# Kernel optimization log

Hardware: AMD Instinct MI355X
Metric: run time of the kernel (lower is better)

The kernel has to match this reference:

```python
import jax, jax.numpy as jnp
import numpy as np

B, N, D, E = 128, 512, 256, 8192  # graphs, nodes/graph, embed_dim, edges/graph
K = int(np.ceil(0.8 * N))         # TopKPooling ratio=0.8 -> k per graph


def setup_inputs() -> dict:
    key = jax.random.key(0)
    ks = jax.random.split(key, 16)
    Ntot = B * N
    x = jax.random.normal(ks[0], (Ntot, 4), jnp.float32)
    offs = (jnp.arange(B, dtype=jnp.int32) * N)[:, None]
    src = (jax.random.randint(ks[1], (B, E), 0, N, jnp.int32) + offs).reshape(-1)
    dst = (jax.random.randint(ks[2], (B, E), 0, N, jnp.int32) + offs).reshape(-1)
    s = 0.05
    w = lambda k, shape: jax.random.normal(k, shape, jnp.float32) * s
    return {
        'x': x, 'src': src, 'dst': dst,
        'Wr1': w(ks[3], (4, D)), 'Ws1': w(ks[4], (4, D)), 'b1': jnp.zeros((D,), jnp.float32),
        'Wr2': w(ks[5], (D, D)), 'Ws2': w(ks[6], (D, D)), 'b2': jnp.zeros((D,), jnp.float32),
        'Wr3': w(ks[7], (D, D)), 'Ws3': w(ks[8], (D, D)), 'b3': jnp.zeros((D,), jnp.float32),
        'p_attn': w(ks[9], (D,)),
        'W1': w(ks[10], (2 * D, D)), 'c1': jnp.zeros((D,), jnp.float32),
        'W2': w(ks[11], (D, D // 2)), 'c2': jnp.zeros((D // 2,), jnp.float32),
        'W3': w(ks[12], (D // 2, 1)), 'c3': jnp.zeros((1,), jnp.float32),
    }


def _graph_conv(x, src, dst, Wr, Ws, b):
    # PyG GraphConv, aggr='add': out = lin_rel(sum_{j in N(i)} x_j) + lin_root(x_i)
    agg = jax.ops.segment_sum(x[src], dst, num_segments=B * N)
    return agg @ Wr + b + x @ Ws


def _gmp_gap(xb):
    # xb: [B, n, D] -> concat(global max pool, global mean pool): [B, 2D]
    return jnp.concatenate([xb.max(axis=1), xb.mean(axis=1)], axis=1)


def reference(x, src, dst, Wr1, Ws1, b1, Wr2, Ws2, b2, Wr3, Ws3, b3,
              p_attn, W1, c1, W2, c2, W3, c3):
    h = jax.nn.relu(_graph_conv(x, src, dst, Wr1, Ws1, b1))
    x1 = _gmp_gap(h.reshape(B, N, D))
    h = jax.nn.relu(_graph_conv(h, src, dst, Wr2, Ws2, b2))
    x2 = _gmp_gap(h.reshape(B, N, D))
    h = jax.nn.relu(_graph_conv(h, src, dst, Wr3, Ws3, b3))
    # TopKPooling: score = x.p/||p||; keep top-k per graph; scale by tanh(score)
    score = (h @ p_attn) / (jnp.linalg.norm(p_attn) + 1e-16)
    vals, idx = jax.lax.top_k(score.reshape(B, N), K)           # [B, K]
    hb = h.reshape(B, N, D)
    sel = jnp.take_along_axis(hb, idx[:, :, None], axis=1) * jnp.tanh(vals)[:, :, None]
    x3 = _gmp_gap(sel)
    z = x1 + x2 + x3
    z = jax.nn.relu(z @ W1 + c1)
    z = jax.nn.relu(z @ W2 + c2)  # dropout is identity in eval mode
    return jax.nn.sigmoid(z @ W3 + c3)[:, 0]
```

## Files before the change

### kernel.cpp

```cpp
#include <hip/hip_runtime.h>

typedef unsigned short u16;
typedef unsigned int u32;

#define B_GRAPHS 128
#define N_NODES  512
#define D_DIM    256
#define E_EDGES  8192
#define K_TOP    410
#define CSR_STRIDE 12288
#define AS 132

typedef __attribute__((ext_vector_type(8))) __bf16 bf16x8;
typedef __attribute__((ext_vector_type(4))) float  f32x4;

__device__ __forceinline__ float bf2f(u16 h) {
  union { u32 u; float f; } c; c.u = ((u32)h) << 16; return c.f;
}
__device__ __forceinline__ float u2f(u32 u) {
  union { u32 u; float f; } c; c.u = u; return c.f;
}
__device__ __forceinline__ u16 f2bf(float f) {
  union { float f; u32 u; } c; c.f = f;
  u32 u = c.u;
  u += 0x7fffu + ((u >> 16) & 1u);
  return (u16)(u >> 16);
}
__device__ __forceinline__ void async_copy16(const void* g, void* l) {
  __builtin_amdgcn_global_load_lds((const __attribute__((address_space(1))) void*)g,
                                   (__attribute__((address_space(3))) void*)l, 16, 0, 0);
}

__global__ void zero_kernel(float* __restrict__ p) {
  *(float4*)&p[(size_t)(blockIdx.x * 256 + threadIdx.x) * 4] = float4{0.f, 0.f, 0.f, 0.f};
}

__global__ void prep_kernel(const float* __restrict__ Wr2, const float* __restrict__ Ws2,
                            const float* __restrict__ Wr3, const float* __restrict__ Ws3,
                            u16* __restrict__ WT) {
  const int mat = blockIdx.y;
  const int n = blockIdx.x;
  const int k = threadIdx.x;
  const float* W = (mat == 0) ? Wr2 : (mat == 1) ? Ws2 : (mat == 2) ? Wr3 : Ws3;
  WT[((size_t)mat << 16) + ((size_t)n << 8) + k] = f2bf(W[(size_t)k * 256 + n]);
}

__global__ __launch_bounds__(256) void csr_kernel(const int* __restrict__ src,
                                                  const int* __restrict__ dst,
                                                  u16* __restrict__ csr_col,
                                                  u32* __restrict__ csr_off) {
  __shared__ u32 cnt[512];
  __shared__ u32 scan[512];
  __shared__ u32 poff[513];
  const int g = blockIdx.x, t = threadIdx.x;
  const int base = g * N_NODES, ebase = g * E_EDGES;
  for (int i = t; i < 512; i += 256) cnt[i] = 0;
  __syncthreads();
  for (int e = t; e < E_EDGES; e += 256)
    atomicAdd(&cnt[dst[ebase + e] - base], 1u);
  __syncthreads();
  for (int i = t; i < 512; i += 256) scan[i] = (cnt[i] + 7u) & ~7u;
  __syncthreads();
  #pragma unroll 1
  for (int d = 1; d < 512; d <<= 1) {
    const u32 v0 = (t >= d) ? scan[t - d] : 0u;
    const u32 v1 = scan[t + 256 - d];
    __syncthreads();
    if (t >= d) scan[t] += v0;
    scan[t + 256] += v1;
    __syncthreads();
  }
  if (t == 0) poff[0] = 0;
  for (int i = t; i < 512; i += 256) poff[i + 1] = scan[i];
  __syncthreads();
  for (int i = t; i < 513; i += 256) csr_off[(size_t)g * 513 + i] = poff[i];
  for (int i = t; i < 512; i += 256) {
    const u32 s = poff[i] + cnt[i], e2 = poff[i + 1];
    for (u32 k = s; k < e2; ++k) csr_col[(size_t)g * CSR_STRIDE + k] = 512;
  }
  __syncthreads();
  for (int i = t; i < 512; i += 256) cnt[i] = poff[i];
  __syncthreads();
  for (int e = t; e < E_EDGES; e += 256) {
    const int d = dst[ebase + e] - base;
    const int s = src[ebase + e] - base;
    const u32 pos = atomicAdd(&cnt[d], 1u);
    csr_col[(size_t)g * CSR_STRIDE + pos] = (u16)s;
  }
}

__global__ __launch_bounds__(256) void conv1_kernel(const float* __restrict__ x,
                             const u16* __restrict__ csr_col, const u32* __restrict__ csr_off,
                             const float* __restrict__ Wr1, const float* __restrict__ Ws1,
                             const float* __restrict__ b1,
                             u16* __restrict__ H1, float* __restrict__ X1) {
  __shared__ float xs[513 * 4];
  __shared__ float aggs[N_NODES * 5];
  __shared__ __align__(16) u16 cols[CSR_STRIDE];
  __shared__ u32 offs[513];
  const int c = blockIdx.x;
  const int g = blockIdx.y;
  const int base = g * N_NODES;
  const int t = threadIdx.x;

  for (int i = t; i < N_NODES; i += 256)
    *(float4*)&xs[i * 4] = *(const float4*)&x[(size_t)(base + i) * 4];
  if (t < 4) xs[512 * 4 + t] = 0.f;
  for (int i = t; i < CSR_STRIDE / 2; i += 256)
    ((u32*)cols)[i] = ((const u32*)(csr_col + (size_t)g * CSR_STRIDE))[i];
  for (int i = t; i < 513; i += 256) offs[i] = csr_off[(size_t)g * 513 + i];
  __syncthreads();

  #pragma unroll
  for (int nn = 0; nn < 2; ++nn) {
    const int i = t * 2 + nn;
    const u32 s0 = offs[i];
    const int nb = (int)((offs[i + 1] - s0) >> 3);
    float a0 = 0.f, a1 = 0.f, a2 = 0.f, a3 = 0.f;
    for (int b = 0; b < nb; ++b) {
      const uint4 cw = *(const uint4*)&cols[s0 + (u32)b * 8];
      const u32 ww[4] = {cw.x, cw.y, cw.z, cw.w};
      #pragma unroll
      for (int q = 0; q < 4; ++q) {
        const int ca = ww[q] & 0xffffu, cb = ww[q] >> 16;
        const float4 va = *(const float4*)&xs[ca * 4];
        const float4 vb = *(const float4*)&xs[cb * 4];
        a0 += va.x + vb.x; a1 += va.y + vb.y;
        a2 += va.z + vb.z; a3 += va.w + vb.w;
      }
    }
    aggs[i * 5 + 0] = a0; aggs[i * 5 + 1] = a1;
    aggs[i * 5 + 2] = a2; aggs[i * 5 + 3] = a3;
  }
  __syncthreads();

  float wr[4], wsv[4];
  #pragma unroll
  for (int k = 0; k < 4; ++k) { wr[k] = Wr1[k * 256 + t]; wsv[k] = Ws1[k * 256 + t]; }
  const float bb = b1[t];
  float mx = 0.f, sm = 0.f;
  const int nlo = c * 256;
  for (int n = nlo; n < nlo + 256; ++n) {
    float acc = bb;
    #pragma unroll
    for (int k = 0; k < 4; ++k) acc += aggs[n * 5 + k] * wr[k] + xs[n * 4 + k] * wsv[k];
    acc = fmaxf(acc, 0.f);
    H1[(size_t)(base + n) * D_DIM + t] = f2bf(acc);
    mx = fmaxf(mx, acc);
    sm += acc;
  }
  atomicMax((int*)&X1[(size_t)g * 512 + t], __float_as_int(mx));
  atomicAdd(&X1[(size_t)g * 512 + 256 + t], sm);
}

__global__ __launch_bounds__(512) void agg_gather_kernel(const u16* __restrict__ H,
                                                         const u16* __restrict__ csr_col,
                                                         const u32* __restrict__ csr_off,
                                                         u16* __restrict__ AGG) {
  __shared__ __align__(16) u16 hs[513 * AS];
  __shared__ __align__(16) u16 cols[CSR_STRIDE + 8];
  __shared__ u32 offs[513];
  const int c = blockIdx.x;
  const int g = blockIdx.y;
  const int base = g * N_NODES;
  const int t = threadIdx.x;

  #pragma unroll
  for (int p = 0; p < 32; ++p) {
    const int flat = p * 512 + t;
    const int row = flat >> 5, q = flat & 31;
    *(uint2*)&hs[row * AS + q * 4] =
        *(const uint2*)&H[(size_t)(base + row) * D_DIM + c * 128 + q * 4];
  }
  if (t < 33) *(uint2*)&hs[512 * AS + t * 4] = uint2{0u, 0u};
  #pragma unroll
  for (int p = 0; p < 12; ++p)
    ((u32*)cols)[p * 512 + t] = ((const u32*)(csr_col + (size_t)g * CSR_STRIDE))[p * 512 + t];
  if (t < 8) cols[CSR_STRIDE + t] = 512;
  for (int i = t; i < 513; i += 512) offs[i] = csr_off[(size_t)g * 513 + i];
  __syncthreads();

  const int w = t >> 6, lane = t & 63;
  const int h2 = lane >> 5, fl = lane & 31;
  const int i0 = w * 64;
  #pragma unroll 1
  for (int j = 0; j < 16; ++j) {
    u32 s0[4]; int nb[4];
    #pragma unroll
    for (int q = 0; q < 4; ++q) {
      const int r = i0 + q * 16 + j;
      s0[q] = offs[r];
      nb[q] = (int)((offs[r + 1] - s0[q]) >> 3);
    }
    const int nbmax = max(max(nb[0], nb[1]), max(nb[2], nb[3]));
    float a[4][4];
    #pragma unroll
    for (int q = 0; q < 4; ++q) { a[q][0] = 0.f; a[q][1] = 0.f; a[q][2] = 0.f; a[q][3] = 0.f; }
    #pragma unroll 1
    for (int b = 0; b < nbmax; ++b) {
      #pragma unroll
      for (int q = 0; q < 4; ++q) {
        const u32 ca = (b < nb[q]) ? (s0[q] + (u32)b * 8u) : (u32)CSR_STRIDE;
        const uint4 cw = *(const uint4*)&cols[ca];
        const u32 w01 = h2 ? cw.z : cw.x;
        const u32 w23 = h2 ? cw.w : cw.y;
        const int c0 = (int)(w01 & 0xffffu), c1 = (int)(w01 >> 16);
        const int c2 = (int)(w23 & 0xffffu), c3 = (int)(w23 >> 16);
        const uint2 d0 = *(const uint2*)&hs[c0 * AS + fl * 4];
        const uint2 d1 = *(const uint2*)&hs[c1 * AS + fl * 4];
        const uint2 d2 = *(const uint2*)&hs[c2 * AS + fl * 4];
        const uint2 d3 = *(const uint2*)&hs[c3 * AS + fl * 4];
        a[q][0] += (u2f(d0.x << 16) + u2f(d1.x << 16)) + (u2f(d2.x << 16) + u2f(d3.x << 16));
        a[q][1] += (u2f(d0.x & 0xffff0000u) + u2f(d1.x & 0xffff0000u))
                 + (u2f(d2.x & 0xffff0000u) + u2f(d3.x & 0xffff0000u));
        a[q][2] += (u2f(d0.y << 16) + u2f(d1.y << 16)) + (u2f(d2.y << 16) + u2f(d3.y << 16));
        a[q][3] += (u2f(d0.y & 0xffff0000u) + u2f(d1.y & 0xffff0000u))
                 + (u2f(d2.y & 0xffff0000u) + u2f(d3.y & 0xffff0000u));
      }
    }
    #pragma unroll
    for (int q = 0; q < 4; ++q) {
      const float r0 = a[q][0] + __shfl_xor(a[q][0], 32);
      const float r1 = a[q][1] + __shfl_xor(a[q][1], 32);
      const float r2 = a[q][2] + __shfl_xor(a[q][2], 32);
      const float r3 = a[q][3] + __shfl_xor(a[q][3], 32);
      if (h2 == 0) {
        uint2 o;
        o.x = (u32)f2bf(r0) | ((u32)f2bf(r1) << 16);
        o.y = (u32)f2bf(r2) | ((u32)f2bf(r3) << 16);
        *(uint2*)&AGG[(size_t)(base + i0 + q * 16 + j) * D_DIM + c * 128 + fl * 4] = o;
      }
    }
  }
}

__global__ __launch_bounds__(256) void gemm_kernel(const u16* __restrict__ Amat,
                                                   const u16* __restrict__ Hmat,
                                                   const u16* __restrict__ WrT,
                                                   const u16* __restrict__ WsT,
                                                   const float* __restrict__ bias,
                                                   u16* __restrict__ Hout,
                                                   float* __restrict__ x2pool,
                                                   float* __restrict__ score,
                                                   const float* __restrict__ pvec) {
  __shared__ __align__(16) u16 At[2][128 * 32];
  __shared__ __align__(16) u16 Bt[2][128 * 32];
  const int m0 = blockIdx.x * 128;
  const int n0 = blockIdx.y * 128;
  const int t = threadIdx.x;
  const int wid = t >> 6, lane = t & 63;
  const int wm = wid >> 1, wn = wid & 1;
  const int r16 = lane & 15, q0 = lane >> 4;

  f32x4 acc[4][4];
  const f32x4 zero = {0.f, 0.f, 0.f, 0.f};
  #pragma unroll
  for (int i = 0; i < 4; ++i)
    #pragma unroll
    for (int jj = 0; jj < 4; ++jj) acc[i][jj] = zero;

  const int srow_off = lane >> 2;
  const int sq = lane & 3;

  auto stage = [&](int s) {
    const int buf = s & 1;
    const int ph = s >> 3;
    const int kk = (s & 7) * 32;
    const u16* Ain = ph ? Hmat : Amat;
    const u16* Win = ph ? WsT : WrT;
    #pragma unroll
    for (int j = 0; j < 4; ++j) {
      const int chk = wid * 4 + j;
      const int ch8 = chk & 7;
      const int r = ch8 * 16 + srow_off;
      const int qsrc = sq ^ ((r >> 1) & 3);
      if (chk < 8)
        async_copy16(&Ain[(size_t)(m0 + r) * 256 + kk + qsrc * 8], &At[buf][ch8 * 512]);
      else
        async_copy16(&Win[(size_t)(n0 + r) * 256 + kk + qsrc * 8], &Bt[buf][ch8 * 512]);
    }
  };

  stage(0);
  #pragma unroll 1
  for (int s = 0; s < 16; ++s) {
    if (s < 15) {
      stage(s + 1);
      asm volatile("s_waitcnt vmcnt(4)" ::: "memory");
    } else {
      asm volatile("s_waitcnt vmcnt(0)" ::: "memory");
    }
    __builtin_amdgcn_s_barrier();
    const int buf = s & 1;
    bf16x8 aF[4], bF[4];
    #pragma unroll
    for (int mi = 0; mi < 4; ++mi) {
      const int arow = wm * 64 + mi * 16 + r16;
      const int qs = q0 ^ ((arow >> 1) & 3);
      aF[mi] = *(const bf16x8*)&At[buf][arow * 32 + qs * 8];
    }
    #pragma unroll
    for (int ni = 0; ni < 4; ++ni) {
      const int brow = wn * 64 + ni * 16 + r16;
      const int qs = q0 ^ ((brow >> 1) & 3);
      bF[ni] = *(const bf16x8*)&Bt[buf][brow * 32 + qs * 8];
    }
    #pragma unroll
    for (int mi = 0; mi < 4; ++mi)
      #pragma unroll
      for (int ni = 0; ni < 4; ++ni)
        acc[mi][ni] = __builtin_amdgcn_mfma_f32_16x16x32_bf16(aF[mi], bF[ni],
                                                              acc[mi][ni], 0, 0, 0);
    __builtin_amdgcn_s_barrier();
  }

  const bool do_x2 = (x2pool != nullptr);
  const bool do_sc = (score != nullptr);
  float colmax[4], colsum[4], pv[4], rpart[4][4];
  #pragma unroll
  for (int ni = 0; ni < 4; ++ni) { colmax[ni] = 0.f; colsum[ni] = 0.f; pv[ni] = 0.f; }
  #pragma unroll
  for (int mi = 0; mi < 4; ++mi)
    #pragma unroll
    for (int r = 0; r < 4; ++r) rpart[mi][r] = 0.f;
  if (do_sc) {
    #pragma unroll
    for (int ni = 0; ni < 4; ++ni) pv[ni] = pvec[n0 + wn * 64 + ni * 16 + r16];
  }

  #pragma unroll
  for (int mi = 0; mi < 4; ++mi) {
    const int growb = m0 + wm * 64 + mi * 16 + q0 * 4;
    #pragma unroll
    for (int ni = 0; ni < 4; ++ni) {
      const int gcol = n0 + wn * 64 + ni * 16 + r16;
      const float bv = bias[gcol];
      #pragma unroll
      for (int r = 0; r < 4; ++r) {
        float v = acc[mi][ni][r] + bv;
        v = fmaxf(v, 0.f);
        Hout[(size_t)(growb + r) * 256 + gcol] = f2bf(v);
        colmax[ni] = fmaxf(colmax[ni], v);
        colsum[ni] += v;
        rpart[mi][r] += v * pv[ni];
      }
    }
  }

  const int gg = m0 >> 9;
  if (do_x2) {
    #pragma unroll
    for (int ni = 0; ni < 4; ++ni) {
      const int gcol = n0 + wn * 64 + ni * 16 + r16;
      float cm = colmax[ni], cs = colsum[ni];
      cm = fmaxf(cm, __shfl_xor(cm, 16));
      cm = fmaxf(cm, __shfl_xor(cm, 32));
      cs += __shfl_xor(cs, 16);
      cs += __shfl_xor(cs, 32);
      if (q0 == 0) {
        atomicMax((int*)&x2pool[(size_t)gg * 512 + gcol], __float_as_int(cm));
        atomicAdd(&x2pool[(size_t)gg * 512 + 256 + gcol], cs);
      }
    }
  }
  if (do_sc) {
    #pragma unroll
    for (int mi = 0; mi < 4; ++mi) {
      const int growb = m0 + wm * 64 + mi * 16 + q0 * 4;
      #pragma unroll
      for (int r = 0; r < 4; ++r) {
        float sp = rpart[mi][r];
        sp += __shfl_xor(sp, 1);
        sp += __shfl_xor(sp, 2);
        sp += __shfl_xor(sp, 4);
        sp += __shfl_xor(sp, 8);
        if (r16 == 0) atomicAdd(&score[growb + r], sp);
      }
    }
  }
}

__global__ __launch_bounds__(256) void sort_kernel(const float* __restrict__ score,
                                                   const float* __restrict__ p,
                                                   u16* __restrict__ top_idx,
                                                   float* __restrict__ top_scale) {
  __shared__ float sval[N_NODES];
  __shared__ int sidx[N_NODES];
  __shared__ float wsum[4];
  const int g = blockIdx.x, t = threadIdx.x;

  float pvt = p[t];
  float sq2 = pvt * pvt;
  #pragma unroll
  for (int off = 32; off > 0; off >>= 1) sq2 += __shfl_down(sq2, off);
  if ((t & 63) == 0) wsum[t >> 6] = sq2;
  __syncthreads();
  const float inv_pn = 1.f / (sqrtf(wsum[0] + wsum[1] + wsum[2] + wsum[3]) + 1e-16f);

  for (int n = t; n < N_NODES; n += 256) {
    sval[n] = score[(size_t)g * 512 + n] * inv_pn;
    sidx[n] = n;
  }
  __syncthreads();

  for (int k = 2; k <= N_NODES; k <<= 1) {
    for (int jj = k >> 1; jj > 0; jj >>= 1) {
      const int i = ((t & ~(jj - 1)) << 1) | (t & (jj - 1));
      const int ix = i | jj;
      const bool dirDesc = ((i & k) == 0);
      const float vi = sval[i], vx = sval[ix];
      const int ii = sidx[i], ij = sidx[ix];
      const bool iAfter = (vi < vx) || (vi == vx && ii > ij);
      if (dirDesc ? iAfter : !iAfter) {
        sval[i] = vx; sval[ix] = vi;
        sidx[i] = ij; sidx[ix] = ii;
      }
      __syncthreads();
    }
  }

  for (int s = t; s < K_TOP; s += 256) {
    top_idx[(size_t)g * 416 + s] = (u16)sidx[s];
    top_scale[(size_t)g * 416 + s] = tanhf(sval[s]);
  }
}

__global__ __launch_bounds__(256) void x3_pool_kernel(const u16* __restrict__ H3,
                                                      const u16* __restrict__ top_idx,
                                                      const float* __restrict__ top_scale,
                                                      float* __restrict__ X3) {
  __shared__ u16 sidxL[416];
  __shared__ float ssclL[416];
  __shared__ float redm[32 * 65];
  __shared__ float reds[32 * 65];
  const int c = blockIdx.x;
  const int g = blockIdx.y;
  const int t = threadIdx.x;
  const int fl = t & 7, rg = t >> 3;

  for (int s = t; s < K_TOP; s += 256) {
    sidxL[s] = top_idx[(size_t)g * 416 + s];
    ssclL[s] = top_scale[(size_t)g * 416 + s];
  }
  __syncthreads();

  float mx[8], sm[8];
  #pragma unroll
  for (int j = 0; j < 8; ++j) { mx[j] = -1e30f; sm[j] = 0.f; }
  const size_t rowbase = (size_t)g * 512;
  for (int s = rg; s < K_TOP; s += 32) {
    const int row = sidxL[s];
    const float sc = ssclL[s];
    const uint4 d = *(const uint4*)&H3[(rowbase + row) * 256 + c * 64 + fl * 8];
    const u32 wv[4] = {d.x, d.y, d.z, d.w};
    #pragma unroll
    for (int q = 0; q < 4; ++q) {
      const float v0 = u2f(wv[q] << 16) * sc;
      const float v1 = u2f(wv[q] & 0xffff0000u) * sc;
      mx[q * 2] = fmaxf(mx[q * 2], v0); sm[q * 2] += v0;
      mx[q * 2 + 1] = fmaxf(mx[q * 2 + 1], v1); sm[q * 2 + 1] += v1;
    }
  }
  #pragma unroll
  for (int j = 0; j < 8; ++j) {
    redm[rg * 65 + fl * 8 + j] = mx[j];
    reds[rg * 65 + fl * 8 + j] = sm[j];
  }
  __syncthreads();
  for (int st = 16; st >= 1; st >>= 1) {
    if (rg < st) {
      #pragma unroll
      for (int j = 0; j < 8; ++j) {
        const int a = rg * 65 + fl * 8 + j, b = (rg + st) * 65 + fl * 8 + j;
        redm[a] = fmaxf(redm[a], redm[b]);
        reds[a] += reds[b];
      }
    }
    __syncthreads();
  }
  if (rg == 0) {
    #pragma unroll
    for (int j = 0; j < 8; ++j) {
      X3[(size_t)g * 512 + c * 64 + fl * 8 + j] = redm[fl * 8 + j];
      X3[(size_t)g * 512 + 256 + c * 64 + fl * 8 + j] = reds[fl * 8 + j] * (1.f / (float)K_TOP);
    }
  }
}

__global__ void mlp_kernel(const float* __restrict__ X1, const float* __restrict__ X2,
                           const float* __restrict__ X3,
                           const float* __restrict__ W1, const float* __restrict__ c1,
                           const float* __restrict__ W2, const float* __restrict__ c2,
                           const float* __restrict__ W3, const float* __restrict__ c3,
                           float* __restrict__ out) {
  __shared__ float zs[512];
  __shared__ float z1[256];
  __shared__ float z2[128];
  const int g = blockIdx.x, t = threadIdx.x;
  for (int k = t; k < 512; k += 256) {
    const float x1v = X1[(size_t)g * 512 + k];
    const float x2v = X2[(size_t)g * 512 + k];
    const float x3v = X3[(size_t)g * 512 + k];
    zs[k] = (k < 256) ? (x1v + x2v + x3v)
                      : (x1v * (1.f / 512.f) + x2v * (1.f / 512.f) + x3v);
  }
  __syncthreads();
  {
    float acc = c1[t];
    for (int k = 0; k < 512; ++k) acc += zs[k] * W1[(size_t)k * 256 + t];
    z1[t] = fmaxf(acc, 0.f);
  }
  __syncthreads();
  if (t < 128) {
    float acc = c2[t];
    for (int d = 0; d < 256; ++d) acc += z1[d] * W2[(size_t)d * 128 + t];
    z2[t] = fmaxf(acc, 0.f);
  }
  __syncthreads();
  if (t == 0) {
    float acc = c3[0];
    for (int e = 0; e < 128; ++e) acc += z2[e] * W3[e];
    out[g] = 1.f / (1.f + expf(-acc));
  }
}

extern "C" void kernel_launch(void* const* d_in, const int* in_sizes, int n_in,
                              void* d_out, int out_size, void* d_ws, size_t ws_size,
                              hipStream_t stream) {
  (void)in_sizes; (void)n_in; (void)out_size; (void)ws_size;
  const float* x   = (const float*)d_in[0];
  const int* src   = (const int*)d_in[1];
  const int* dstp  = (const int*)d_in[2];
  const float* Wr1 = (const float*)d_in[3];
  const float* Ws1 = (const float*)d_in[4];
  const float* b1  = (const float*)d_in[5];
  const float* Wr2 = (const float*)d_in[6];
  const float* Ws2 = (const float*)d_in[7];
  const float* b2  = (const float*)d_in[8];
  const float* Wr3 = (const float*)d_in[9];
  const float* Ws3 = (const float*)d_in[10];
  const float* b3  = (const float*)d_in[11];
  const float* pat = (const float*)d_in[12];
  const float* W1  = (const float*)d_in[13];
  const float* c1  = (const float*)d_in[14];
  const float* W2  = (const float*)d_in[15];
  const float* c2  = (const float*)d_in[16];
  const float* W3  = (const float*)d_in[17];
  const float* c3  = (const float*)d_in[18];
  float* out = (float*)d_out;

  char* ws = (char*)d_ws;
  u16* hA  = (u16*)(ws);
  u16* hB  = (u16*)(ws + 33554432);
  u16* AGG = (u16*)(ws + 67108864);
  u16* WT  = (u16*)(ws + 100663296);
  float* x1 = (float*)(ws + 101187584);
  float* x2 = (float*)(ws + 101449728);
  float* x3 = (float*)(ws + 101711872);
  u16* csr_col = (u16*)(ws + 101974016);
  u32* csr_off = (u32*)(ws + 105119744);
  float* score     = (float*)(ws + 101974016);
  u16* top_idx     = (u16*)(ws + 101974016 + 262144);
  float* top_scale = (float*)(ws + 101974016 + 372736);

  prep_kernel<<<dim3(256, 4), dim3(256), 0, stream>>>(Wr2, Ws2, Wr3, Ws3, WT);
  csr_kernel<<<dim3(128), dim3(256), 0, stream>>>(src, dstp, csr_col, csr_off);
  zero_kernel<<<dim3(128), dim3(256), 0, stream>>>(x1);
  conv1_kernel<<<dim3(2, 128), dim3(256), 0, stream>>>(x, csr_col, csr_off, Wr1, Ws1, b1, hA, x1);

  agg_gather_kernel<<<dim3(2, 128), dim3(512), 0, stream>>>(hA, csr_col, csr_off, AGG);
  gemm_kernel<<<dim3(512, 2), dim3(256), 0, stream>>>(AGG, hA, WT, WT + 65536, b2, hB,
                                                      x2, nullptr, nullptr);

  agg_gather_kernel<<<dim3(2, 128), dim3(512), 0, stream>>>(hB, csr_col, csr_off, AGG);
  zero_kernel<<<dim3(64), dim3(256), 0, stream>>>(score);
  gemm_kernel<<<dim3(512, 2), dim3(256), 0, stream>>>(AGG, hB, WT + 131072, WT + 196608, b3, hA,
                                                      nullptr, score, pat);

  sort_kernel<<<dim3(128), dim3(256), 0, stream>>>(score, pat, top_idx, top_scale);
  x3_pool_kernel<<<dim3(4, 128), dim3(256), 0, stream>>>(hA, top_idx, top_scale, x3);
  mlp_kernel<<<dim3(128), dim3(256), 0, stream>>>(x1, x2, x3, W1, c1, W2, c2, W3, c3, out);
}
```

Measured before the change: 267.1 us.

## Sort rows by degree per wave and prescale CSR column indices

CSR column entries now hold the source index premultiplied by 33 (AS/4), so the gather computes LDS addresses with a single add and shift instead of a multiply. conv1 decodes the index with a multiply-shift. Each wave bitonic-sorts its 64 rows by block count so the four rows handled together have similar degree, which cuts idle iterations from degree imbalance. The column buffer is shrunk to fit alongside the new sort workspace. This relies on the maximum padded edge count per graph fitting within LCOL, an assumption about the input distribution.

```diff
diff --git a/kernel.cpp b/kernel.cpp
--- a/kernel.cpp
+++ b/kernel.cpp
@@ -9,6 +9,7 @@
 #define E_EDGES  8192
 #define K_TOP    410
 #define CSR_STRIDE 12288
+#define LCOL 11792
 #define AS 132
 
 typedef __attribute__((ext_vector_type(8))) __bf16 bf16x8;
@@ -76,7 +77,7 @@
   for (int i = t; i < 513; i += 256) csr_off[(size_t)g * 513 + i] = poff[i];
   for (int i = t; i < 512; i += 256) {
     const u32 s = poff[i] + cnt[i], e2 = poff[i + 1];
-    for (u32 k = s; k < e2; ++k) csr_col[(size_t)g * CSR_STRIDE + k] = 512;
+    for (u32 k = s; k < e2; ++k) csr_col[(size_t)g * CSR_STRIDE + k] = 16896;
   }
   __syncthreads();
   for (int i = t; i < 512; i += 256) cnt[i] = poff[i];
@@ -85,7 +86,7 @@
     const int d = dst[ebase + e] - base;
     const int s = src[ebase + e] - base;
     const u32 pos = atomicAdd(&cnt[d], 1u);
-    csr_col[(size_t)g * CSR_STRIDE + pos] = (u16)s;
+    csr_col[(size_t)g * CSR_STRIDE + pos] = (u16)(s * 33);
   }
 }
 
@@ -122,7 +123,8 @@
       const u32 ww[4] = {cw.x, cw.y, cw.z, cw.w};
       #pragma unroll
       for (int q = 0; q < 4; ++q) {
-        const int ca = ww[q] & 0xffffu, cb = ww[q] >> 16;
+        const int ca = (int)(((ww[q] & 0xffffu) * 63551u) >> 21);
+        const int cb = (int)(((ww[q] >> 16) * 63551u) >> 21);
         const float4 va = *(const float4*)&xs[ca * 4];
         const float4 vb = *(const float4*)&xs[cb * 4];
         a0 += va.x + vb.x; a1 += va.y + vb.y;
@@ -158,8 +160,9 @@
                                                          const u32* __restrict__ csr_off,
                                                          u16* __restrict__ AGG) {
   __shared__ __align__(16) u16 hs[513 * AS];
-  __shared__ __align__(16) u16 cols[CSR_STRIDE + 8];
+  __shared__ __align__(16) u16 cols[LCOL];
   __shared__ u32 offs[513];
+  __shared__ u32 swork[512];
   const int c = blockIdx.x;
   const int g = blockIdx.y;
   const int base = g * N_NODES;
@@ -173,43 +176,72 @@
         *(const uint2*)&H[(size_t)(base + row) * D_DIM + c * 128 + q * 4];
   }
   if (t < 33) *(uint2*)&hs[512 * AS + t * 4] = uint2{0u, 0u};
-  #pragma unroll
-  for (int p = 0; p < 12; ++p)
-    ((u32*)cols)[p * 512 + t] = ((const u32*)(csr_col + (size_t)g * CSR_STRIDE))[p * 512 + t];
-  if (t < 8) cols[CSR_STRIDE + t] = 512;
+  {
+    const u32* colsw = (const u32*)(csr_col + (size_t)g * CSR_STRIDE);
+    #pragma unroll
+    for (int p = 0; p < 12; ++p) {
+      const int i = p * 512 + t;
+      if (i < (LCOL - 8) / 2) ((u32*)cols)[i] = colsw[i];
+    }
+  }
+  if (t < 8) cols[LCOL - 8 + t] = 16896;
   for (int i = t; i < 513; i += 512) offs[i] = csr_off[(size_t)g * 513 + i];
   __syncthreads();
 
   const int w = t >> 6, lane = t & 63;
+  {
+    const int row = (w << 6) + lane;
+    const u32 s0 = offs[row];
+    const u32 nb = (offs[row + 1] - s0) >> 3;
+    u32 key = (nb << 16) | (u32)row;
+    #pragma unroll
+    for (int k = 2; k <= 64; k <<= 1) {
+      #pragma unroll
+      for (int jj = k >> 1; jj > 0; jj >>= 1) {
+        const u32 o = (u32)__shfl_xor((int)key, jj);
+        const bool up = ((lane & k) == 0);
+        const bool lower = ((lane & jj) == 0);
+        const u32 mn = min(key, o), mx = max(key, o);
+        key = (up == lower) ? mn : mx;
+      }
+    }
+    swork[(w << 6) + lane] = key;
+  }
+  __syncthreads();
+
   const int h2 = lane >> 5, fl = lane & 31;
-  const int i0 = w * 64;
+  const int i0w = w << 6;
+  const u32 padu = (u32)(LCOL - 8 + h2 * 4);
+  const u32 h2o = (u32)(h2 * 4);
   #pragma unroll 1
   for (int j = 0; j < 16; ++j) {
-    u32 s0[4]; int nb[4];
-    #pragma unroll
-    for (int q = 0; q < 4; ++q) {
-      const int r = i0 + q * 16 + j;
-      s0[q] = offs[r];
-      nb[q] = (int)((offs[r + 1] - s0[q]) >> 3);
-    }
-    const int nbmax = max(max(nb[0], nb[1]), max(nb[2], nb[3]));
+    const uint4 kw = *(const uint4*)&swork[i0w + j * 4];
+    const int r0 = (int)(kw.x & 0xffffu), r1 = (int)(kw.y & 0xffffu);
+    const int r2 = (int)(kw.z & 0xffffu), r3 = (int)(kw.w & 0xffffu);
+    const int n0b = (int)(kw.x >> 16), n1b = (int)(kw.y >> 16);
+    const int n2b = (int)(kw.z >> 16), n3b = (int)(kw.w >> 16);
+    const int nbmax = n3b;
+    u32 cu0 = offs[r0] + h2o, cu1 = offs[r1] + h2o;
+    u32 cu2 = offs[r2] + h2o, cu3 = offs[r3] + h2o;
     float a[4][4];
     #pragma unroll
     for (int q = 0; q < 4; ++q) { a[q][0] = 0.f; a[q][1] = 0.f; a[q][2] = 0.f; a[q][3] = 0.f; }
     #pragma unroll 1
     for (int b = 0; b < nbmax; ++b) {
+      const u32 u0 = (b < n0b) ? cu0 : padu;
+      const u32 u1 = (b < n1b) ? cu1 : padu;
+      const u32 u2 = (b < n2b) ? cu2 : padu;
+      const u32 u3 = (b < n3b) ? cu3 : padu;
+      const u32 uu[4] = {u0, u1, u2, u3};
       #pragma unroll
       for (int q = 0; q < 4; ++q) {
-        const u32 ca = (b < nb[q]) ? (s0[q] + (u32)b * 8u) : (u32)CSR_STRIDE;
-        const uint4 cw = *(const uint4*)&cols[ca];
-        const u32 w01 = h2 ? cw.z : cw.x;
-        const u32 w23 = h2 ? cw.w : cw.y;
-        const int c0 = (int)(w01 & 0xffffu), c1 = (int)(w01 >> 16);
-        const int c2 = (int)(w23 & 0xffffu), c3 = (int)(w23 >> 16);
-        const uint2 d0 = *(const uint2*)&hs[c0 * AS + fl * 4];
-        const uint2 d1 = *(const uint2*)&hs[c1 * AS + fl * 4];
-        const uint2 d2 = *(const uint2*)&hs[c2 * AS + fl * 4];
-        const uint2 d3 = *(const uint2*)&hs[c3 * AS + fl * 4];
+        const uint2 cw = *(const uint2*)&cols[uu[q]];
+        const int e0 = (int)(cw.x & 0xffffu), e1 = (int)(cw.x >> 16);
+        const int e2 = (int)(cw.y & 0xffffu), e3 = (int)(cw.y >> 16);
+        const uint2 d0 = *(const uint2*)&hs[(u32)(e0 + fl) << 2];
+        const uint2 d1 = *(const uint2*)&hs[(u32)(e1 + fl) << 2];
+        const uint2 d2 = *(const uint2*)&hs[(u32)(e2 + fl) << 2];
+        const uint2 d3 = *(const uint2*)&hs[(u32)(e3 + fl) << 2];
         a[q][0] += (u2f(d0.x << 16) + u2f(d1.x << 16)) + (u2f(d2.x << 16) + u2f(d3.x << 16));
         a[q][1] += (u2f(d0.x & 0xffff0000u) + u2f(d1.x & 0xffff0000u))
                  + (u2f(d2.x & 0xffff0000u) + u2f(d3.x & 0xffff0000u));
@@ -217,18 +249,20 @@
         a[q][3] += (u2f(d0.y & 0xffff0000u) + u2f(d1.y & 0xffff0000u))
                  + (u2f(d2.y & 0xffff0000u) + u2f(d3.y & 0xffff0000u));
       }
-    }
+      cu0 += 8; cu1 += 8; cu2 += 8; cu3 += 8;
+    }
+    const int rw[4] = {r0, r1, r2, r3};
     #pragma unroll
     for (int q = 0; q < 4; ++q) {
-      const float r0 = a[q][0] + __shfl_xor(a[q][0], 32);
-      const float r1 = a[q][1] + __shfl_xor(a[q][1], 32);
-      const float r2 = a[q][2] + __shfl_xor(a[q][2], 32);
-      const float r3 = a[q][3] + __shfl_xor(a[q][3], 32);
+      const float v0 = a[q][0] + __shfl_xor(a[q][0], 32);
+      const float v1 = a[q][1] + __shfl_xor(a[q][1], 32);
+      const float v2 = a[q][2] + __shfl_xor(a[q][2], 32);
+      const float v3 = a[q][3] + __shfl_xor(a[q][3], 32);
       if (h2 == 0) {
         uint2 o;
-        o.x = (u32)f2bf(r0) | ((u32)f2bf(r1) << 16);
-        o.y = (u32)f2bf(r2) | ((u32)f2bf(r3) << 16);
-        *(uint2*)&AGG[(size_t)(base + i0 + q * 16 + j) * D_DIM + c * 128 + fl * 4] = o;
+        o.x = (u32)f2bf(v0) | ((u32)f2bf(v1) << 16);
+        o.y = (u32)f2bf(v2) | ((u32)f2bf(v3) << 16);
+        *(uint2*)&AGG[(size_t)(base + rw[q]) * D_DIM + c * 128 + fl * 4] = o;
       }
     }
   }
```

Measured after the change: 255.0 us. 1.05x faster.
